# Optimization experiments

Hardware: AMD Instinct MI355X
Metric: run time of the kernel (lower is better)

Reference implementation:

```python
import jax, jax.numpy as jnp
import numpy as np

HID = 16  # module-level output_size constant
D = 64    # input_dim
K = 32    # number of classes / outer nets
B = 8192  # batch


def setup_inputs() -> dict:
    key = jax.random.key(0)
    ks = jax.random.split(key, 9)
    s = 0.1
    return {
        "x": jax.random.normal(ks[0], (B, D), dtype=jnp.float32),
        # inner nets: one tiny 1->16->1 MLP per (k, i)
        "iw1": jax.random.normal(ks[1], (K, D, HID), dtype=jnp.float32) * s,  # Linear(1,16) weight
        "ib1": jax.random.normal(ks[2], (K, D, HID), dtype=jnp.float32) * s,  # Linear(1,16) bias
        "iw2": jax.random.normal(ks[3], (K, D, HID), dtype=jnp.float32) * s,  # Linear(16,1) weight
        "ib2": jax.random.normal(ks[4], (K, D), dtype=jnp.float32) * s,       # Linear(16,1) bias
        # outer nets: one 1->16->1 MLP per k
        "ow1": jax.random.normal(ks[5], (K, HID), dtype=jnp.float32) * s,
        "ob1": jax.random.normal(ks[6], (K, HID), dtype=jnp.float32) * s,
        "ow2": jax.random.normal(ks[7], (K, HID), dtype=jnp.float32) * s,
        "ob2": jax.random.normal(ks[8], (K,), dtype=jnp.float32) * s,
    }


def reference(x, iw1, ib1, iw2, ib2, ow1, ob1, ow2, ob2):
    # Inner nets, all K*D at once. Linear(1,HID) on scalar xi is an outer product.
    # h: [B, K, D, HID]
    h = jax.nn.relu(x[:, None, :, None] * iw1[None] + ib1[None])
    # Linear(HID,1): contract HID -> yi: [B, K, D]
    yi = jnp.einsum('bkdh,kdh->bkd', h, iw2) + ib2[None]
    # sum over input features i -> [B, K]
    sk = yi.sum(axis=2)
    # Outer nets: scalar -> HID -> scalar per k
    g = jax.nn.relu(sk[:, :, None] * ow1[None] + ob1[None])  # [B, K, HID]
    out = jnp.einsum('bkh,kh->bk', g, ow2) + ob2[None]       # [B, K]
    return out
```

## Files before the change

kernel.cpp:

```cpp
#include <hip/hip_runtime.h>
#include <hip/hip_bf16.h>

#define HID 16
#define DIN 64
#define NK  32
#define NB  8192

typedef float v4f __attribute__((ext_vector_type(4)));

struct PW {
    float A, B;
    float u[HID];
    float c[HID];
};

__device__ __forceinline__ float pl_eval(const PW& w, float xd) {
    float a0 = fmaf(w.A, xd, w.B);
    float a1 = 0.f;
    #pragma unroll
    for (int h = 0; h < HID; h += 2) {
        const float t0 = xd + w.c[h];
        const float t1 = xd + w.c[h + 1];
        a0 = fmaf(fabsf(t0), w.u[h],     a0);
        a1 = fmaf(fabsf(t1), w.u[h + 1], a1);
    }
    return a0 + a1;
}

__global__ __launch_bounds__(256, 4) void kan_kernel(
    const float* __restrict__ x,
    const float* __restrict__ iw1, const float* __restrict__ ib1,
    const float* __restrict__ iw2, const float* __restrict__ ib2,
    const float* __restrict__ ow1, const float* __restrict__ ob1,
    const float* __restrict__ ow2, const float* __restrict__ ob2,
    float* __restrict__ out)
{
    __shared__ float lds[4][DIN * 17];

    const int t    = threadIdx.x;
    const int lane = t & 63;
    const int wid  = t >> 6;
    const int k    = blockIdx.x & (NK - 1);
    const int base = ((blockIdx.x >> 5) * 4 + wid) * 64;

    PW w;
    {
        v4f w1v[4], b1v[4], w2v[4];
        const v4f* p1 = (const v4f*)(iw1 + (k * DIN + lane) * HID);
        const v4f* p2 = (const v4f*)(ib1 + (k * DIN + lane) * HID);
        const v4f* p3 = (const v4f*)(iw2 + (k * DIN + lane) * HID);
        #pragma unroll
        for (int q = 0; q < 4; ++q) { w1v[q] = p1[q]; b1v[q] = p2[q]; w2v[q] = p3[q]; }

        float A = 0.f;
        float B = ib2[k * DIN + lane];
        #pragma unroll
        for (int h = 0; h < HID; ++h) {
            const float w1  = w1v[h >> 2][h & 3];
            const float b1  = b1v[h >> 2][h & 3];
            const float w2h = w2v[h >> 2][h & 3];
            A = fmaf(0.5f * w2h, w1, A);
            B = fmaf(0.5f * w2h, b1, B);
            const float aw = fabsf(w1);
            const bool ok  = aw > 1e-20f;
            w.c[h] = ok ? b1 * __builtin_amdgcn_rcpf(w1) : 0.f;
            w.u[h] = ok ? 0.5f * w2h * aw : 0.f;
            if (!ok) B = fmaf(0.5f * w2h, fabsf(b1), B);
        }
        w.A = A; w.B = B;
    }

    float* __restrict__ myLds = lds[wid];
    const float* __restrict__ xp = x + base * DIN + lane;

    const int jj  = lane & 15;
    const int pmy = lane >> 4;
    float* __restrict__ wb = myLds + lane * 17;
    const float* __restrict__ rb = myLds + (pmy * 16) * 17 + jj;

    float xr[16];
    const float* __restrict__ xq = xp;
    #pragma unroll
    for (int j = 0; j < 16; ++j) xr[j] = xq[j * DIN];
    xq += 16 * DIN;

    float sk = 0.f;

    #pragma clang loop unroll(disable)
    for (int p = 0; p < 4; ++p) {
        #pragma unroll
        for (int j = 0; j < 16; ++j) wb[j] = pl_eval(w, xr[j]);
        if (p < 3) {
            #pragma unroll
            for (int j = 0; j < 16; ++j) xr[j] = xq[j * DIN];
            xq += 16 * DIN;
        }
        float s = 0.f;
        #pragma unroll
        for (int i = 0; i < 16; ++i) s += rb[i * 17];
        s += __shfl_xor(s, 16, 64);
        s += __shfl_xor(s, 32, 64);
        sk = (p == pmy) ? s : sk;
    }

    float o = ob2[k];
    #pragma unroll
    for (int h = 0; h < HID; ++h) {
        const float g = fmaxf(fmaf(sk, ow1[k * HID + h], ob1[k * HID + h]), 0.f);
        o = fmaf(g, ow2[k * HID + h], o);
    }

    out[(base + lane) * NK + k] = o;
}

extern "C" void kernel_launch(void* const* d_in, const int* in_sizes, int n_in,
                              void* d_out, int out_size, void* d_ws, size_t ws_size,
                              hipStream_t stream) {
    const float* x   = (const float*)d_in[0];
    const float* iw1 = (const float*)d_in[1];
    const float* ib1 = (const float*)d_in[2];
    const float* iw2 = (const float*)d_in[3];
    const float* ib2 = (const float*)d_in[4];
    const float* ow1 = (const float*)d_in[5];
    const float* ob1 = (const float*)d_in[6];
    const float* ow2 = (const float*)d_in[7];
    const float* ob2 = (const float*)d_in[8];
    float* out = (float*)d_out;

    const int grid = (NB / 256) * NK;
    kan_kernel<<<grid, 256, 0, stream>>>(x, iw1, ib1, iw2, ib2,
                                         ow1, ob1, ow2, ob2, out);
}
```

Before: 27.08 us.

## Fully unroll phase loop with double-buffered LDS and two x register sets

Replaces the rolled 4-phase loop with a fully unrolled schedule. It uses two LDS buffers per wave and two register sets for x rows, so global loads for later phases are issued earlier and the LDS reduction of one phase overlaps with evaluation of the next. The 16-term serial reduction sum becomes a tree sum for more ILP. This adds register pressure (32 x values plus a 16-value reduction array) and doubles LDS use, which could hurt occupancy under launch_bounds(256,4).

Result: no change. 26.84 us (-0.9%).

```diff
diff --git a/kernel.cpp b/kernel.cpp
--- a/kernel.cpp
+++ b/kernel.cpp
@@ -35,7 +35,7 @@
     const float* __restrict__ ow2, const float* __restrict__ ob2,
     float* __restrict__ out)
 {
-    __shared__ float lds[4][DIN * 17];
+    __shared__ float lds[4][2][DIN * 17];
 
     const int t    = threadIdx.x;
     const int lane = t & 63;
@@ -70,38 +70,58 @@
         w.A = A; w.B = B;
     }
 
-    float* __restrict__ myLds = lds[wid];
     const float* __restrict__ xp = x + base * DIN + lane;
 
     const int jj  = lane & 15;
-    const int pmy = lane >> 4;
-    float* __restrict__ wb = myLds + lane * 17;
-    const float* __restrict__ rb = myLds + (pmy * 16) * 17 + jj;
+    const int pgr = lane >> 4;
 
-    float xr[16];
-    const float* __restrict__ xq = xp;
+    float* __restrict__ wb0 = &lds[wid][0][lane * 17];
+    float* __restrict__ wb1 = &lds[wid][1][lane * 17];
+    const float* __restrict__ rb0 = &lds[wid][0][(pgr * 16) * 17 + jj];
+    const float* __restrict__ rb1 = &lds[wid][1][(pgr * 16) * 17 + jj];
+
+    float xa[16], xb[16];
+    float rsum[4];
+
     #pragma unroll
-    for (int j = 0; j < 16; ++j) xr[j] = xq[j * DIN];
-    xq += 16 * DIN;
+    for (int j = 0; j < 16; ++j) xa[j] = xp[(0 * 16 + j) * DIN];
+    #pragma unroll
+    for (int j = 0; j < 16; ++j) xb[j] = xp[(1 * 16 + j) * DIN];
 
-    float sk = 0.f;
+    #pragma unroll
+    for (int j = 0; j < 16; ++j) wb0[j] = pl_eval(w, xa[j]);
+    #pragma unroll
+    for (int j = 0; j < 16; ++j) xa[j] = xp[(2 * 16 + j) * DIN];
+    #pragma unroll
+    for (int j = 0; j < 16; ++j) wb1[j] = pl_eval(w, xb[j]);
+    #pragma unroll
+    for (int j = 0; j < 16; ++j) xb[j] = xp[(3 * 16 + j) * DIN];
 
-    #pragma clang loop unroll(disable)
-    for (int p = 0; p < 4; ++p) {
+    auto reduce = [&](const float* rb) -> float {
+        float v[16];
         #pragma unroll
-        for (int j = 0; j < 16; ++j) wb[j] = pl_eval(w, xr[j]);
-        if (p < 3) {
+        for (int i = 0; i < 16; ++i) v[i] = rb[i * 17];
+        #pragma unroll
+        for (int m = 8; m; m >>= 1)
             #pragma unroll
-            for (int j = 0; j < 16; ++j) xr[j] = xq[j * DIN];
-            xq += 16 * DIN;
-        }
-        float s = 0.f;
-        #pragma unroll
-        for (int i = 0; i < 16; ++i) s += rb[i * 17];
+            for (int i = 0; i < m; ++i) v[i] += v[i + m];
+        float s = v[0];
         s += __shfl_xor(s, 16, 64);
         s += __shfl_xor(s, 32, 64);
-        sk = (p == pmy) ? s : sk;
-    }
+        return s;
+    };
+
+    rsum[0] = reduce(rb0);
+    #pragma unroll
+    for (int j = 0; j < 16; ++j) wb0[j] = pl_eval(w, xa[j]);
+    rsum[1] = reduce(rb1);
+    #pragma unroll
+    for (int j = 0; j < 16; ++j) wb1[j] = pl_eval(w, xb[j]);
+    rsum[2] = reduce(rb0);
+    rsum[3] = reduce(rb1);
+
+    const float sk = (lane & 32) ? ((lane & 16) ? rsum[3] : rsum[2])
+                                 : ((lane & 16) ? rsum[1] : rsum[0]);
 
     float o = ob2[k];
     #pragma unroll
```
